# Kernel tuning notes

Hardware: AMD Instinct MI355X
Metric: run time of the kernel (lower is better)

## Reference

```python
import jax, jax.numpy as jnp
import numpy as np

H = 16       # num heads
D = 80       # head dim
HID = H * D  # 1280
S = 4096     # total tokens


def setup_inputs() -> dict:
    key = jax.random.key(0)
    ks = jax.random.split(key, 6)
    x = jax.random.normal(ks[0], (S, HID), dtype=jnp.float32)
    # 4 images of 1024 patch tokens each
    cu_seqlens = jnp.array([0, 1024, 2048, 3072, 4096], dtype=jnp.int32)
    rotary_pos_emb = jax.random.normal(ks[1], (S, D // 2), dtype=jnp.float32)
    sc = 1.0 / np.sqrt(HID)
    qkv_w = jax.random.normal(ks[2], (3 * HID, HID), dtype=jnp.float32) * sc
    qkv_b = jax.random.normal(ks[3], (3 * HID,), dtype=jnp.float32) * 0.02
    proj_w = jax.random.normal(ks[4], (HID, HID), dtype=jnp.float32) * sc
    proj_b = jax.random.normal(ks[5], (HID,), dtype=jnp.float32) * 0.02
    return {"x": x, "cu_seqlens": cu_seqlens, "rotary_pos_emb": rotary_pos_emb,
            "qkv_w": qkv_w, "qkv_b": qkv_b, "proj_w": proj_w, "proj_b": proj_b}


def _rotate_half(t):
    t1, t2 = jnp.split(t, 2, axis=-1)
    return jnp.concatenate([-t2, t1], axis=-1)


def _apply_rope(t, freqs):
    # t: [S, H, D], freqs: [S, D//2] -> cos/sin broadcast as [S, 1, D]
    emb = jnp.concatenate([freqs, freqs], axis=-1)[:, None, :]
    return t * jnp.cos(emb) + _rotate_half(t) * jnp.sin(emb)


def reference(x, cu_seqlens, rotary_pos_emb, qkv_w, qkv_b, proj_w, proj_b):
    seq_len = x.shape[0]
    qkv = (x @ qkv_w.T + qkv_b).reshape(seq_len, 3, H, D)
    q, k, v = qkv[:, 0], qkv[:, 1], qkv[:, 2]  # each [S, H, D]
    q = _apply_rope(q, rotary_pos_emb)
    k = _apply_rope(k, rotary_pos_emb)
    # block-diagonal mask from cu_seqlens: same segment -> 0, else dtype min
    seg = jnp.searchsorted(cu_seqlens[1:], jnp.arange(seq_len), side='right')
    neg = jnp.finfo(q.dtype).min
    attn_mask = jnp.where(seg[:, None] == seg[None, :], 0.0, neg).astype(q.dtype)
    scores = jnp.einsum('shd,thd->hst', q, k) / jnp.sqrt(jnp.asarray(D, q.dtype))
    scores = scores + attn_mask[None]
    attn = jax.nn.softmax(scores.astype(jnp.float32), axis=-1).astype(q.dtype)
    out = jnp.einsum('hst,thd->shd', attn, v).reshape(seq_len, H * D)
    return out @ proj_w.T + proj_b
```

## Files before the change

### kernel.cpp

```cpp
#include <hip/hip_runtime.h>

typedef _Float16 f16;
typedef __attribute__((ext_vector_type(8))) _Float16 f16x8;
typedef __attribute__((ext_vector_type(4))) float f32x4;

#define SEQ   4096
#define NH    16
#define HD    80
#define HIDN  1280
#define DP    96

#define KSZ   3328
#define VSZ   4480
#define HSZ   (2*KSZ + 2*VSZ)

#define KQ   1280
#define NQ   3840
#define NIT  10

__device__ __forceinline__ void gload16(const void* g, void* l) {
  __builtin_amdgcn_global_load_lds(
      (const __attribute__((address_space(1))) unsigned int*)g,
      (__attribute__((address_space(3))) unsigned int*)l, 16, 0, 0);
}

__device__ __forceinline__ f16x8 bc16(uint4 u) { return __builtin_bit_cast(f16x8, u); }
__device__ __forceinline__ unsigned pk2(float a, float b) {
  return __builtin_bit_cast(unsigned, __builtin_amdgcn_cvt_pkrtz(a, b));
}

#define BAR() __builtin_amdgcn_s_barrier()
#define VMCNT(n) do { asm volatile("s_waitcnt vmcnt(" #n ")" ::: "memory"); \
                      __builtin_amdgcn_sched_barrier(0); } while (0)
#define STG(Lb, g, buf, h, kt)                                                  \
  do {                                                                          \
    gload16((g) + (size_t)((h) * 128) * KQ + (kt) * 64,                         \
            (Lb) + (buf) * 16384 + ((h) * 128) * 64 + w * 512);                 \
    gload16((g) + (size_t)((h) * 128 + 64) * KQ + (kt) * 64,                    \
            (Lb) + (buf) * 16384 + ((h) * 128 + 64) * 64 + w * 512);            \
  } while (0)
#define MFQ(IOFF, JOFF, BB)                                                     \
  do {                                                                          \
    __builtin_amdgcn_s_setprio(1);                                              \
    _Pragma("unroll")                                                           \
    for (int i_ = 0; i_ < 4; i_++)                                              \
      _Pragma("unroll")                                                         \
      for (int j_ = 0; j_ < 2; j_++)                                            \
        _Pragma("unroll")                                                       \
        for (int s_ = 0; s_ < 2; s_++)                                          \
          acc[i_ + IOFF][j_ + JOFF] = __builtin_amdgcn_mfma_f32_16x16x32_f16(   \
              a[i_][s_], BB[j_][s_], acc[i_ + IOFF][j_ + JOFF], 0, 0, 0);       \
    __builtin_amdgcn_s_setprio(0);                                              \
  } while (0)

__global__ __launch_bounds__(256) void cvt3_kernel(const float* __restrict__ s0,
                                                   const float* __restrict__ s1,
                                                   const float* __restrict__ s2,
                                                   f16* __restrict__ d0,
                                                   f16* __restrict__ d1,
                                                   f16* __restrict__ d2,
                                                   int n0, int n1, int n2) {
  long i = (long)(blockIdx.x * 256 + threadIdx.x) * 8;
  const float* s; f16* d;
  if (i < n0)                { s = s0 + i;            d = d0 + i; }
  else if (i < n0 + n1)      { s = s1 + (i - n0);     d = d1 + (i - n0); }
  else if (i < n0 + n1 + n2) { s = s2 + (i - n0 - n1); d = d2 + (i - n0 - n1); }
  else return;
  f32x4 v0 = *(const f32x4*)(s);
  f32x4 v1 = *(const f32x4*)(s + 4);
  f16x8 o;
#pragma unroll
  for (int j = 0; j < 4; j++) { o[j] = (f16)v0[j]; o[4 + j] = (f16)v1[j]; }
  *(f16x8*)(d) = o;
}

__global__ __launch_bounds__(512, 2) void qkv_gemm8(const f16* __restrict__ A,
                                                    const f16* __restrict__ B,
                                                    const float* __restrict__ bias,
                                                    f16* __restrict__ C) {
  __shared__ __align__(16) f16 LA[2 * 16384];
  __shared__ __align__(16) f16 LB[2 * 16384];
  const int tid = threadIdx.x, w = tid >> 6, l = tid & 63;
  const int bid = (blockIdx.x & 7) * 30 + (blockIdx.x >> 3);
  const int bx = bid % 15, by = bid / 15;
  const int m0 = by * 256, n0 = bx * 256;
  const int wm = (w >> 2) * 128, wn = (w & 3) * 64;
  const int fr = l & 15, fq = l >> 4;
  const int rx = fr & 7;
  const int cA0 = (fq ^ rx) * 8;
  const int cA1 = ((4 + fq) ^ rx) * 8;

  const int srow = w * 8 + (l >> 3);
  const int scol = ((l & 7) ^ (l >> 3)) * 8;
  const f16* gA = A + (size_t)(m0 + srow) * KQ + scol;
  const f16* gB = B + (size_t)(n0 + srow) * KQ + scol;

  f32x4 acc[8][4] = {};
  f16x8 a[4][2], b0[2][2], b1[2][2];

  STG(LA, gA, 0, 0, 0); STG(LA, gA, 0, 1, 0);
  STG(LB, gB, 0, 0, 0); STG(LB, gB, 0, 1, 0);
  STG(LB, gB, 1, 0, 1); STG(LB, gB, 1, 1, 1);
  VMCNT(4);
  BAR();

  for (int it = 0; it < NIT; ++it) {
    const int t = 2 * it;
    const bool lastit = (it == NIT - 1);

#pragma unroll
    for (int i = 0; i < 4; i++) {
      a[i][0] = *(const f16x8*)(LA + (wm + i * 16 + fr) * 64 + cA0);
      a[i][1] = *(const f16x8*)(LA + (wm + i * 16 + fr) * 64 + cA1);
    }
#pragma unroll
    for (int j = 0; j < 2; j++) {
      b0[j][0] = *(const f16x8*)(LB + (wn + j * 16 + fr) * 64 + cA0);
      b0[j][1] = *(const f16x8*)(LB + (wn + j * 16 + fr) * 64 + cA1);
    }
    STG(LA, gA, 1, 0, t + 1);
    BAR(); MFQ(0, 0, b0); BAR();

#pragma unroll
    for (int j = 0; j < 2; j++) {
      b1[j][0] = *(const f16x8*)(LB + (wn + 32 + j * 16 + fr) * 64 + cA0);
      b1[j][1] = *(const f16x8*)(LB + (wn + 32 + j * 16 + fr) * 64 + cA1);
    }
    STG(LA, gA, 1, 1, t + 1);
    BAR(); MFQ(0, 2, b1); BAR();

#pragma unroll
    for (int i = 0; i < 4; i++) {
      a[i][0] = *(const f16x8*)(LA + (wm + 64 + i * 16 + fr) * 64 + cA0);
      a[i][1] = *(const f16x8*)(LA + (wm + 64 + i * 16 + fr) * 64 + cA1);
    }
    if (!lastit) { STG(LB, gB, 0, 0, t + 2); }
    BAR(); MFQ(4, 0, b0); BAR();

    if (!lastit) { STG(LB, gB, 0, 1, t + 2); VMCNT(4); }
    else         { VMCNT(0); }
    BAR(); MFQ(4, 2, b1); BAR();

#pragma unroll
    for (int i = 0; i < 4; i++) {
      a[i][0] = *(const f16x8*)(LA + 16384 + (wm + i * 16 + fr) * 64 + cA0);
      a[i][1] = *(const f16x8*)(LA + 16384 + (wm + i * 16 + fr) * 64 + cA1);
    }
#pragma unroll
    for (int j = 0; j < 2; j++) {
      b0[j][0] = *(const f16x8*)(LB + 16384 + (wn + j * 16 + fr) * 64 + cA0);
      b0[j][1] = *(const f16x8*)(LB + 16384 + (wn + j * 16 + fr) * 64 + cA1);
    }
    if (!lastit) { STG(LA, gA, 0, 0, t + 2); }
    BAR(); MFQ(0, 0, b0); BAR();

#pragma unroll
    for (int j = 0; j < 2; j++) {
      b1[j][0] = *(const f16x8*)(LB + 16384 + (wn + 32 + j * 16 + fr) * 64 + cA0);
      b1[j][1] = *(const f16x8*)(LB + 16384 + (wn + 32 + j * 16 + fr) * 64 + cA1);
    }
    if (!lastit) { STG(LA, gA, 0, 1, t + 2); }
    BAR(); MFQ(0, 2, b1); BAR();

#pragma unroll
    for (int i = 0; i < 4; i++) {
      a[i][0] = *(const f16x8*)(LA + 16384 + (wm + 64 + i * 16 + fr) * 64 + cA0);
      a[i][1] = *(const f16x8*)(LA + 16384 + (wm + 64 + i * 16 + fr) * 64 + cA1);
    }
    if (!lastit) { STG(LB, gB, 1, 0, t + 3); }
    BAR(); MFQ(4, 0, b0); BAR();

    if (!lastit) { STG(LB, gB, 1, 1, t + 3); VMCNT(4); }
    BAR(); MFQ(4, 2, b1); BAR();
  }

#pragma unroll
  for (int i = 0; i < 8; i++) {
    const int row = m0 + wm + i * 16 + fq * 4;
#pragma unroll
    for (int j = 0; j < 4; j++) {
      const int col = n0 + wn + j * 16 + fr;
      const float bv = bias[col];
#pragma unroll
      for (int q = 0; q < 4; q++)
        C[(size_t)(row + q) * NQ + col] = (f16)(acc[i][j][q] + bv);
    }
  }
}

template<int OUT_F32>
__global__ __launch_bounds__(256) void gemm_bt(const f16* __restrict__ A,
                                               const f16* __restrict__ B,
                                               const float* __restrict__ bias,
                                               void* __restrict__ C,
                                               int M, int N, int K) {
  __shared__ __align__(16) f16 As[128 * 32];
  __shared__ __align__(16) f16 Bs[128 * 32];
  const int tid = threadIdx.x;
  const int w = tid >> 6, l = tid & 63;
  const int m0 = blockIdx.y * 128, n0 = blockIdx.x * 128;
  const int wm = (w >> 1) * 64, wn = (w & 1) * 64;

  const int c0 = w * 64 + l;
  const int c1 = (4 + w) * 64 + l;
  const size_t a0 = (size_t)(m0 + (c0 >> 2)) * K + (c0 & 3) * 8;
  const size_t a1 = (size_t)(m0 + (c1 >> 2)) * K + (c1 & 3) * 8;
  const size_t b0 = (size_t)(n0 + (c0 >> 2)) * K + (c0 & 3) * 8;
  const size_t b1 = (size_t)(n0 + (c1 >> 2)) * K + (c1 & 3) * 8;

  f32x4 acc[4][4] = {};
  const int fr = l & 15, fg = (l >> 4) * 8;

  for (int k0 = 0; k0 < K; k0 += 32) {
    if (k0) __syncthreads();
    gload16(A + a0 + k0, As + w * 512);
    gload16(A + a1 + k0, As + (4 + w) * 512);
    gload16(B + b0 + k0, Bs + w * 512);
    gload16(B + b1 + k0, Bs + (4 + w) * 512);
    __syncthreads();
    f16x8 af[4], bf[4];
#pragma unroll
    for (int i = 0; i < 4; i++)
      af[i] = *(const f16x8*)(As + (wm + i * 16 + fr) * 32 + fg);
#pragma unroll
    for (int j = 0; j < 4; j++)
      bf[j] = *(const f16x8*)(Bs + (wn + j * 16 + fr) * 32 + fg);
#pragma unroll
    for (int i = 0; i < 4; i++)
#pragma unroll
      for (int j = 0; j < 4; j++)
        acc[i][j] = __builtin_amdgcn_mfma_f32_16x16x32_f16(af[i], bf[j], acc[i][j], 0, 0, 0);
  }

  const int q4 = (l >> 4) * 4;
#pragma unroll
  for (int i = 0; i < 4; i++) {
    const int row = m0 + wm + i * 16 + q4;
#pragma unroll
    for (int j = 0; j < 4; j++) {
      const int col = n0 + wn + j * 16 + fr;
      const float bv = bias[col];
#pragma unroll
      for (int q = 0; q < 4; q++) {
        float v = acc[i][j][q] + bv;
        if (OUT_F32) ((float*)C)[(size_t)(row + q) * N + col] = v;
        else         ((f16*)C)[(size_t)(row + q) * N + col] = (f16)v;
      }
    }
  }
}

__global__ __launch_bounds__(256) void rope_kernel(const f16* __restrict__ qkvb,
                                                   const float* __restrict__ rpe,
                                                   f16* __restrict__ qh,
                                                   f16* __restrict__ kh) {
  const float SCLT = 0.1118033988749895f * 1.4426950408889634f;
  int t = blockIdx.x * 256 + threadIdx.x;
  if (t >= SEQ * NH * 40) return;
  const int d = t % 40;
  const int h = (t / 40) % NH;
  const int s = t / (40 * NH);
  const float f = rpe[s * 40 + d];
  float sn, cs;
  __sincosf(f, &sn, &cs);
  const size_t base = (size_t)s * (3 * HIDN) + h * HD;
  const float q0 = (float)qkvb[base + d];
  const float q1 = (float)qkvb[base + 40 + d];
  const float k0 = (float)qkvb[base + HIDN + d];
  const float k1 = (float)qkvb[base + HIDN + 40 + d];
  const size_t ob = ((size_t)h * SEQ + s) * DP;
  qh[ob + d]      = (f16)((q0 * cs - q1 * sn) * SCLT);
  qh[ob + 40 + d] = (f16)((q1 * cs + q0 * sn) * SCLT);
  kh[ob + d]      = (f16)(k0 * cs - k1 * sn);
  kh[ob + 40 + d] = (f16)(k1 * cs + k0 * sn);
  if (d < DP - HD) { qh[ob + HD + d] = (f16)0.f; kh[ob + HD + d] = (f16)0.f; }
}

__global__ __launch_bounds__(256) void vtrans_kernel(const f16* __restrict__ qkvb,
                                                     f16* __restrict__ vt) {
  __shared__ f16 tile[HD][65];
  const int h = blockIdx.y;
  const int s0 = blockIdx.x * 64;
  for (int idx = threadIdx.x; idx < 64 * HD; idx += 256) {
    const int sr = idx / HD, d = idx % HD;
    tile[d][sr] = qkvb[(size_t)(s0 + sr) * (3 * HIDN) + 2 * HIDN + h * HD + d];
  }
  __syncthreads();
  for (int idx = threadIdx.x; idx < HD * 64; idx += 256) {
    const int d = idx >> 6, sc = idx & 63;
    const int b = sc >> 5, s = sc & 31, g = s >> 3, j = s & 7;
    const int act = b * 32 + ((j < 4) ? (4 * g + j) : (16 + 4 * g + (j - 4)));
    vt[((size_t)h * HD + d) * SEQ + s0 + sc] = tile[d][act];
  }
}

__global__ __launch_bounds__(512, 4) void attn_kernel(const f16* __restrict__ qh,
                                                      const f16* __restrict__ kh,
                                                      const f16* __restrict__ vt,
                                                      const int* __restrict__ cu,
                                                      f16* __restrict__ ao) {
  __shared__ __align__(16) f16 smem[2 * HSZ];
  const int tid = threadIdx.x, w = tid >> 6, l = tid & 63;
  const int grp = w >> 2, wq = w & 3;
  const int h = blockIdx.y;
  const int qblk = blockIdx.x * 128;
  int seg = 0;
  while (cu[seg + 1] <= qblk) seg++;
  const int kvb = cu[seg], kve = cu[seg + 1];
  const int nt = (kve - kvb + 63) >> 6;
  const int fr = l & 15, fg = (l >> 4) * 8;
  const int row0 = qblk + wq * 32;

  const f16* qb = qh + ((size_t)h * SEQ + row0 + fr) * DP + fg;
  f16x8 aq0[3], aq1[3];
#pragma unroll
  for (int kk = 0; kk < 3; kk++) {
    aq0[kk] = *(const f16x8*)(qb + kk * 32);
    aq1[kk] = *(const f16x8*)(qb + 16 * DP + kk * 32);
  }

  const int k0g = tid / 384, k0r = (tid % 384) / 12, k0c = tid % 12;
  const int k1r = (128 + tid) / 12, k1c = (128 + tid) % 12;
  const int v0g = tid / 320, v0r = (tid % 320) / 4, v0c = tid & 3;
  const int v1r = (192 + tid) >> 2, v1c = (192 + tid) & 3;
  const f16* kp0 = kh + ((size_t)h * SEQ + kvb + k0g * 32 + k0r) * DP + k0c * 8;
  const f16* kp1 = kh + ((size_t)h * SEQ + kvb + 32 + k1r) * DP + k1c * 8;
  const f16* vp0 = vt + ((size_t)h * HD + v0r) * SEQ + kvb + v0g * 32 + v0c * 8;
  const f16* vp1 = vt + ((size_t)h * HD + v1r) * SEQ + kvb + 32 + v1c * 8;
  const int dK0 = k0g * KSZ + k0r * 104 + k0c * 8;
  const int dK1 = KSZ + k1r * 104 + k1c * 8;
  const int dV0 = 2 * KSZ + v0g * VSZ + v0r * 56 + v0c * 8;
  const int dV1 = 2 * KSZ + VSZ + v1r * 56 + v1c * 8;

  float m = -1e30f, ls0 = 0.f, ls1 = 0.f;
  f32x4 o0[5] = {}, o1[5] = {};

  uint4 rk0, rk1, rv0, rv1;
  rk0 = *(const uint4*)kp0;
  if (tid < 256) rk1 = *(const uint4*)kp1;
  rv0 = *(const uint4*)vp0;
  if (tid < 128) rv1 = *(const uint4*)vp1;
  *(uint4*)(smem + dK0) = rk0;
  if (tid < 256) *(uint4*)(smem + dK1) = rk1;
  *(uint4*)(smem + dV0) = rv0;
  if (tid < 128) *(uint4*)(smem + dV1) = rv1;
  __syncthreads();

  for (int t = 0; t < nt; t++) {
    const int p = t & 1;
    const int off = (t + 1) * 64;
    const bool more = (t + 1 < nt);

    if (more) {
      rk0 = *(const uint4*)(kp0 + (size_t)off * DP);
      if (tid < 256) rk1 = *(const uint4*)(kp1 + (size_t)off * DP);
      rv0 = *(const uint4*)(vp0 + off);
      if (tid < 128) rv1 = *(const uint4*)(vp1 + off);
    }

    const f16* myK = smem + p * HSZ + grp * KSZ;
    const f16* myV = smem + p * HSZ + 2 * KSZ + grp * VSZ;

    f32x4 s00 = {0.f,0.f,0.f,0.f}, s10 = {0.f,0.f,0.f,0.f};
    f32x4 s01 = {0.f,0.f,0.f,0.f}, s11 = {0.f,0.f,0.f,0.f};
    __builtin_amdgcn_s_setprio(1);
#pragma unroll
    for (int kk = 0; kk < 3; kk++) {
      const f16x8 k0 = *(const f16x8*)(myK + fr * 104 + kk * 32 + fg);
      const f16x8 k1 = *(const f16x8*)(myK + (16 + fr) * 104 + kk * 32 + fg);
      s00 = __builtin_amdgcn_mfma_f32_16x16x32_f16(k0, aq0[kk], s00, 0, 0, 0);
      s10 = __builtin_amdgcn_mfma_f32_16x16x32_f16(k1, aq0[kk], s10, 0, 0, 0);
      s01 = __builtin_amdgcn_mfma_f32_16x16x32_f16(k0, aq1[kk], s01, 0, 0, 0);
      s11 = __builtin_amdgcn_mfma_f32_16x16x32_f16(k1, aq1[kk], s11, 0, 0, 0);
    }
    __builtin_amdgcn_s_setprio(0);

    float pmax = fmaxf(fmaxf(s00[0], s10[0]), fmaxf(s01[0], s11[0]));
#pragma unroll
    for (int j = 1; j < 4; j++) {
      pmax = fmaxf(pmax, fmaxf(s00[j], s10[j]));
      pmax = fmaxf(pmax, fmaxf(s01[j], s11[j]));
    }
    if (__any(pmax > m + 8.f)) {
      float tmax = pmax;
      tmax = fmaxf(tmax, __shfl_xor(tmax, 1));
      tmax = fmaxf(tmax, __shfl_xor(tmax, 2));
      tmax = fmaxf(tmax, __shfl_xor(tmax, 4));
      tmax = fmaxf(tmax, __shfl_xor(tmax, 8));
      tmax = fmaxf(tmax, __shfl_xor(tmax, 16));
      tmax = fmaxf(tmax, __shfl_xor(tmax, 32));
      const float aa = __builtin_amdgcn_exp2f(m - tmax);
      m = tmax;
      ls0 *= aa; ls1 *= aa;
#pragma unroll
      for (int dt = 0; dt < 5; dt++)
#pragma unroll
        for (int j = 0; j < 4; j++) { o0[dt][j] *= aa; o1[dt][j] *= aa; }
    }

#pragma unroll
    for (int r = 0; r < 4; r++) {
      s00[r] = __builtin_amdgcn_exp2f(s00[r] - m);
      s10[r] = __builtin_amdgcn_exp2f(s10[r] - m);
      s01[r] = __builtin_amdgcn_exp2f(s01[r] - m);
      s11[r] = __builtin_amdgcn_exp2f(s11[r] - m);
      ls0 += s00[r] + s10[r];
      ls1 += s01[r] + s11[r];
    }
    uint4 ua, ub;
    ua.x = pk2(s00[0], s00[1]); ua.y = pk2(s00[2], s00[3]);
    ua.z = pk2(s10[0], s10[1]); ua.w = pk2(s10[2], s10[3]);
    ub.x = pk2(s01[0], s01[1]); ub.y = pk2(s01[2], s01[3]);
    ub.z = pk2(s11[0], s11[1]); ub.w = pk2(s11[2], s11[3]);
    const f16x8 paA = bc16(ua), paB = bc16(ub);

    __builtin_amdgcn_s_setprio(1);
#pragma unroll
    for (int dt = 0; dt < 5; dt++) {
      const f16x8 bv = *(const f16x8*)(myV + (dt * 16 + fr) * 56 + fg);
      o0[dt] = __builtin_amdgcn_mfma_f32_16x16x32_f16(paA, bv, o0[dt], 0, 0, 0);
      o1[dt] = __builtin_amdgcn_mfma_f32_16x16x32_f16(paB, bv, o1[dt], 0, 0, 0);
    }
    __builtin_amdgcn_s_setprio(0);

    if (more) {
      f16* dst = smem + (1 - p) * HSZ;
      *(uint4*)(dst + dK0) = rk0;
      if (tid < 256) *(uint4*)(dst + dK1) = rk1;
      *(uint4*)(dst + dV0) = rv0;
      if (tid < 128) *(uint4*)(dst + dV1) = rv1;
    }
    __syncthreads();
  }

  ls0 += __shfl_xor(ls0, 16); ls0 += __shfl_xor(ls0, 32);
  ls1 += __shfl_xor(ls1, 16); ls1 += __shfl_xor(ls1, 32);

  float* mb = (float*)smem;
  if (grp == 1) {
    float* dst = mb + (wq * 64 + l) * 43;
    dst[0] = m; dst[1] = ls0; dst[2] = ls1;
#pragma unroll
    for (int dt = 0; dt < 5; dt++)
#pragma unroll
      for (int j = 0; j < 4; j++) {
        dst[3 + dt * 4 + j]  = o0[dt][j];
        dst[23 + dt * 4 + j] = o1[dt][j];
      }
  }
  __syncthreads();
  if (grp == 0) {
    const float* src = mb + (wq * 64 + l) * 43;
    const float mB = src[0];
    const float M = fmaxf(m, mB);
    const float aA = __builtin_amdgcn_exp2f(m - M);
    const float aB = __builtin_amdgcn_exp2f(mB - M);
    ls0 = ls0 * aA + src[1] * aB;
    ls1 = ls1 * aA + src[2] * aB;
#pragma unroll
    for (int dt = 0; dt < 5; dt++)
#pragma unroll
      for (int j = 0; j < 4; j++) {
        o0[dt][j] = o0[dt][j] * aA + src[3 + dt * 4 + j] * aB;
        o1[dt][j] = o1[dt][j] * aA + src[23 + dt * 4 + j] * aB;
      }

    const float inv0 = 1.0f / ls0, inv1 = 1.0f / ls1;
    float iv0[4], iv1[4];
#pragma unroll
    for (int j = 0; j < 4; j++) {
      const int srcl = (l & 48) | ((l >> 4) * 4 + j);
      iv0[j] = __shfl(inv0, srcl);
      iv1[j] = __shfl(inv1, srcl);
    }
    const int orow = row0 + (l >> 4) * 4;
#pragma unroll
    for (int dt = 0; dt < 5; dt++)
#pragma unroll
      for (int j = 0; j < 4; j++) {
        ao[(size_t)(orow + j) * HIDN + h * HD + dt * 16 + fr]      = (f16)(o0[dt][j] * iv0[j]);
        ao[(size_t)(orow + 16 + j) * HIDN + h * HD + dt * 16 + fr] = (f16)(o1[dt][j] * iv1[j]);
      }
  }
}

extern "C" void kernel_launch(void* const* d_in, const int* in_sizes, int n_in,
                              void* d_out, int out_size, void* d_ws, size_t ws_size,
                              hipStream_t stream) {
  const float* x      = (const float*)d_in[0];
  const int*   cu     = (const int*)d_in[1];
  const float* rpe    = (const float*)d_in[2];
  const float* qkv_w  = (const float*)d_in[3];
  const float* qkv_b  = (const float*)d_in[4];
  const float* proj_w = (const float*)d_in[5];
  const float* proj_b = (const float*)d_in[6];

  char* ws = (char*)d_ws;
  f16* xb    = (f16*)(ws);
  f16* wqkv  = (f16*)(ws + 10485760);
  f16* wproj = (f16*)(ws + 20316160);
  f16* qkvb  = (f16*)(ws + 23592960);
  f16* qh    = (f16*)(ws + 55050240);
  f16* kh    = (f16*)(ws + 67633152);
  f16* vt    = (f16*)(ws + 80216064);
  f16* ao    = xb;

  const int n0 = SEQ * HIDN, n1 = 3 * HIDN * HIDN, n2 = HIDN * HIDN;
  cvt3_kernel<<<(n0 + n1 + n2) / (256 * 8), 256, 0, stream>>>(
      x, qkv_w, proj_w, xb, wqkv, wproj, n0, n1, n2);

  qkv_gemm8<<<240, 512, 0, stream>>>(xb, wqkv, qkv_b, qkvb);

  rope_kernel<<<(SEQ * NH * 40) / 256, 256, 0, stream>>>(qkvb, rpe, qh, kh);
  vtrans_kernel<<<dim3(SEQ / 64, NH), 256, 0, stream>>>(qkvb, vt);

  attn_kernel<<<dim3(SEQ / 128, NH), 512, 0, stream>>>(qh, kh, vt, cu, ao);

  gemm_bt<1><<<dim3(HIDN / 128, SEQ / 128), 256, 0, stream>>>(
      ao, wproj, proj_b, d_out, SEQ, HIDN, HIDN);
}
```

Baseline: 154.3 us.

## Widen attention to three KV groups with async LDS loads, fuse rope/vtrans, deepen proj GEMM K-tile

The attention kernel moves from 2 to 3 key/value groups (768 threads, 96-key tiles) and stages K/V straight into LDS with global_load_lds instead of register round-trips. The three partial softmax states are then merged in two phases. RoPE and the V transpose are fused into one prep kernel with vectorized 8-wide rope, and the output projection GEMM now loads 64-wide K slices per barrier. The goal is fewer launches, fewer barriers and better latency hiding. The costs are a higher register and LDS budget per block, clamped loads on a partial last tile, and a longer merge.

```diff
diff --git a/kernel.cpp b/kernel.cpp
--- a/kernel.cpp
+++ b/kernel.cpp
@@ -10,9 +10,10 @@
 #define HIDN  1280
 #define DP    96
 
-#define KSZ   3328
-#define VSZ   4480
-#define HSZ   (2*KSZ + 2*VSZ)
+#define KTS   3072
+#define VTS   2560
+#define KREG  (3*KTS)
+#define ABUF  (KREG + 3*VTS)
 
 #define KQ   1280
 #define NQ   3840
@@ -24,10 +25,10 @@
       (__attribute__((address_space(3))) unsigned int*)l, 16, 0, 0);
 }
 
-__device__ __forceinline__ f16x8 bc16(uint4 u) { return __builtin_bit_cast(f16x8, u); }
 __device__ __forceinline__ unsigned pk2(float a, float b) {
   return __builtin_bit_cast(unsigned, __builtin_amdgcn_cvt_pkrtz(a, b));
 }
+__device__ __forceinline__ f16x8 bc16(uint4 u) { return __builtin_bit_cast(f16x8, u); }
 
 #define BAR() __builtin_amdgcn_s_barrier()
 #define VMCNT(n) do { asm volatile("s_waitcnt vmcnt(" #n ")" ::: "memory"); \
@@ -189,47 +190,53 @@
 }
 
 template<int OUT_F32>
-__global__ __launch_bounds__(256) void gemm_bt(const f16* __restrict__ A,
-                                               const f16* __restrict__ B,
-                                               const float* __restrict__ bias,
-                                               void* __restrict__ C,
-                                               int M, int N, int K) {
-  __shared__ __align__(16) f16 As[128 * 32];
-  __shared__ __align__(16) f16 Bs[128 * 32];
+__global__ __launch_bounds__(256) void gemm_bt64(const f16* __restrict__ A,
+                                                 const f16* __restrict__ B,
+                                                 const float* __restrict__ bias,
+                                                 void* __restrict__ C,
+                                                 int M, int N, int K) {
+  __shared__ __align__(16) f16 AsF[8192];
+  __shared__ __align__(16) f16 BsF[8192];
   const int tid = threadIdx.x;
   const int w = tid >> 6, l = tid & 63;
   const int m0 = blockIdx.y * 128, n0 = blockIdx.x * 128;
   const int wm = (w >> 1) * 64, wn = (w & 1) * 64;
-
-  const int c0 = w * 64 + l;
-  const int c1 = (4 + w) * 64 + l;
-  const size_t a0 = (size_t)(m0 + (c0 >> 2)) * K + (c0 & 3) * 8;
-  const size_t a1 = (size_t)(m0 + (c1 >> 2)) * K + (c1 & 3) * 8;
-  const size_t b0 = (size_t)(n0 + (c0 >> 2)) * K + (c0 & 3) * 8;
-  const size_t b1 = (size_t)(n0 + (c1 >> 2)) * K + (c1 & 3) * 8;
+  const int fr = l & 15, fg = (l >> 4) * 8;
+
+  size_t aoff[4], boff[4];
+#pragma unroll
+  for (int i = 0; i < 4; i++) {
+    const int d = i * 256 + tid;
+    const int sub = d >> 9, dd = d & 511;
+    const int r = dd >> 2, c = (dd & 3) + sub * 4;
+    aoff[i] = (size_t)(m0 + r) * K + c * 8;
+    boff[i] = (size_t)(n0 + r) * K + c * 8;
+  }
 
   f32x4 acc[4][4] = {};
-  const int fr = l & 15, fg = (l >> 4) * 8;
-
-  for (int k0 = 0; k0 < K; k0 += 32) {
+
+  for (int k0 = 0; k0 < K; k0 += 64) {
     if (k0) __syncthreads();
-    gload16(A + a0 + k0, As + w * 512);
-    gload16(A + a1 + k0, As + (4 + w) * 512);
-    gload16(B + b0 + k0, Bs + w * 512);
-    gload16(B + b1 + k0, Bs + (4 + w) * 512);
+#pragma unroll
+    for (int i = 0; i < 4; i++) gload16(A + aoff[i] + k0, AsF + (i * 256 + tid) * 8);
+#pragma unroll
+    for (int i = 0; i < 4; i++) gload16(B + boff[i] + k0, BsF + (i * 256 + tid) * 8);
     __syncthreads();
-    f16x8 af[4], bf[4];
+    f16x8 af[4][2], bf[4][2];
 #pragma unroll
     for (int i = 0; i < 4; i++)
-      af[i] = *(const f16x8*)(As + (wm + i * 16 + fr) * 32 + fg);
-#pragma unroll
-    for (int j = 0; j < 4; j++)
-      bf[j] = *(const f16x8*)(Bs + (wn + j * 16 + fr) * 32 + fg);
+#pragma unroll
+      for (int s = 0; s < 2; s++) {
+        af[i][s] = *(const f16x8*)(AsF + s * 4096 + (wm + i * 16 + fr) * 32 + fg);
+        bf[i][s] = *(const f16x8*)(BsF + s * 4096 + (wn + i * 16 + fr) * 32 + fg);
+      }
 #pragma unroll
     for (int i = 0; i < 4; i++)
 #pragma unroll
       for (int j = 0; j < 4; j++)
-        acc[i][j] = __builtin_amdgcn_mfma_f32_16x16x32_f16(af[i], bf[j], acc[i][j], 0, 0, 0);
+#pragma unroll
+        for (int s = 0; s < 2; s++)
+          acc[i][j] = __builtin_amdgcn_mfma_f32_16x16x32_f16(af[i][s], bf[j][s], acc[i][j], 0, 0, 0);
   }
 
   const int q4 = (l >> 4) * 4;
@@ -250,56 +257,74 @@
   }
 }
 
-__global__ __launch_bounds__(256) void rope_kernel(const f16* __restrict__ qkvb,
+#define RPB 1280
+__global__ __launch_bounds__(256) void prep_kernel(const f16* __restrict__ qkvb,
                                                    const float* __restrict__ rpe,
                                                    f16* __restrict__ qh,
-                                                   f16* __restrict__ kh) {
-  const float SCLT = 0.1118033988749895f * 1.4426950408889634f;
-  int t = blockIdx.x * 256 + threadIdx.x;
-  if (t >= SEQ * NH * 40) return;
-  const int d = t % 40;
-  const int h = (t / 40) % NH;
-  const int s = t / (40 * NH);
-  const float f = rpe[s * 40 + d];
-  float sn, cs;
-  __sincosf(f, &sn, &cs);
-  const size_t base = (size_t)s * (3 * HIDN) + h * HD;
-  const float q0 = (float)qkvb[base + d];
-  const float q1 = (float)qkvb[base + 40 + d];
-  const float k0 = (float)qkvb[base + HIDN + d];
-  const float k1 = (float)qkvb[base + HIDN + 40 + d];
-  const size_t ob = ((size_t)h * SEQ + s) * DP;
-  qh[ob + d]      = (f16)((q0 * cs - q1 * sn) * SCLT);
-  qh[ob + 40 + d] = (f16)((q1 * cs + q0 * sn) * SCLT);
-  kh[ob + d]      = (f16)(k0 * cs - k1 * sn);
-  kh[ob + 40 + d] = (f16)(k1 * cs + k0 * sn);
-  if (d < DP - HD) { qh[ob + HD + d] = (f16)0.f; kh[ob + HD + d] = (f16)0.f; }
-}
-
-__global__ __launch_bounds__(256) void vtrans_kernel(const f16* __restrict__ qkvb,
-                                                     f16* __restrict__ vt) {
+                                                   f16* __restrict__ kh,
+                                                   f16* __restrict__ vt) {
   __shared__ f16 tile[HD][65];
-  const int h = blockIdx.y;
-  const int s0 = blockIdx.x * 64;
-  for (int idx = threadIdx.x; idx < 64 * HD; idx += 256) {
-    const int sr = idx / HD, d = idx % HD;
-    tile[d][sr] = qkvb[(size_t)(s0 + sr) * (3 * HIDN) + 2 * HIDN + h * HD + d];
-  }
-  __syncthreads();
-  for (int idx = threadIdx.x; idx < HD * 64; idx += 256) {
-    const int d = idx >> 6, sc = idx & 63;
-    const int b = sc >> 5, s = sc & 31, g = s >> 3, j = s & 7;
-    const int act = b * 32 + ((j < 4) ? (4 * g + j) : (16 + 4 * g + (j - 4)));
-    vt[((size_t)h * HD + d) * SEQ + s0 + sc] = tile[d][act];
-  }
-}
-
-__global__ __launch_bounds__(512, 4) void attn_kernel(const f16* __restrict__ qh,
+  const int b = blockIdx.x;
+  if (b < RPB) {
+    const float SCLT = 0.1118033988749895f * 1.4426950408889634f;
+    const int t = b * 256 + threadIdx.x;
+    const int d8 = (t % 5) * 8;
+    const int h = (t / 5) % NH;
+    const int s = t / (5 * NH);
+    const f32x4 f0 = *(const f32x4*)(rpe + s * 40 + d8);
+    const f32x4 f1 = *(const f32x4*)(rpe + s * 40 + d8 + 4);
+    const f16* base = qkvb + (size_t)s * (3 * HIDN) + h * HD;
+    const f16x8 q0 = *(const f16x8*)(base + d8);
+    const f16x8 q1 = *(const f16x8*)(base + 40 + d8);
+    const f16x8 k0 = *(const f16x8*)(base + HIDN + d8);
+    const f16x8 k1 = *(const f16x8*)(base + HIDN + 40 + d8);
+    f16x8 oq0, oq1, ok0, ok1;
+#pragma unroll
+    for (int j = 0; j < 8; j++) {
+      const float fv = (j < 4) ? f0[j] : f1[j - 4];
+      float sn, cs;
+      __sincosf(fv, &sn, &cs);
+      const float a = (float)q0[j], bq = (float)q1[j];
+      oq0[j] = (f16)((a * cs - bq * sn) * SCLT);
+      oq1[j] = (f16)((bq * cs + a * sn) * SCLT);
+      const float ka = (float)k0[j], kb = (float)k1[j];
+      ok0[j] = (f16)(ka * cs - kb * sn);
+      ok1[j] = (f16)(kb * cs + ka * sn);
+    }
+    const size_t ob = ((size_t)h * SEQ + s) * DP;
+    *(f16x8*)(qh + ob + d8)      = oq0;
+    *(f16x8*)(qh + ob + 40 + d8) = oq1;
+    *(f16x8*)(kh + ob + d8)      = ok0;
+    *(f16x8*)(kh + ob + 40 + d8) = ok1;
+    if (d8 == 32) {
+      const f16x8 z = {};
+      *(f16x8*)(qh + ob + 80) = z; *(f16x8*)(qh + ob + 88) = z;
+      *(f16x8*)(kh + ob + 80) = z; *(f16x8*)(kh + ob + 88) = z;
+    }
+  } else {
+    const int bb = b - RPB;
+    const int h = bb >> 6;
+    const int s0 = (bb & 63) * 64;
+    for (int idx = threadIdx.x; idx < 64 * HD; idx += 256) {
+      const int sr = idx / HD, d = idx % HD;
+      tile[d][sr] = qkvb[(size_t)(s0 + sr) * (3 * HIDN) + 2 * HIDN + h * HD + d];
+    }
+    __syncthreads();
+    for (int idx = threadIdx.x; idx < HD * 64; idx += 256) {
+      const int d = idx >> 6, sc = idx & 63;
+      const int blk = sc >> 5, s = sc & 31, g = s >> 3, j = s & 7;
+      const int act = blk * 32 + ((j < 4) ? (4 * g + j) : (16 + 4 * g + (j - 4)));
+      vt[((size_t)h * HD + d) * SEQ + s0 + sc] = tile[d][act];
+    }
+  }
+}
+
+__global__ __launch_bounds__(768, 6) void attn_kernel(const f16* __restrict__ qh,
                                                       const f16* __restrict__ kh,
                                                       const f16* __restrict__ vt,
                                                       const int* __restrict__ cu,
                                                       f16* __restrict__ ao) {
-  __shared__ __align__(16) f16 smem[2 * HSZ];
+  __shared__ __align__(16) f16 smem[2 * ABUF];
   const int tid = threadIdx.x, w = tid >> 6, l = tid & 63;
   const int grp = w >> 2, wq = w & 3;
   const int h = blockIdx.y;
@@ -307,7 +332,7 @@
   int seg = 0;
   while (cu[seg + 1] <= qblk) seg++;
   const int kvb = cu[seg], kve = cu[seg + 1];
-  const int nt = (kve - kvb + 63) >> 6;
+  const int nt = (kve - kvb + 95) / 96;
   const int fr = l & 15, fg = (l >> 4) * 8;
   const int row0 = qblk + wq * 32;
 
@@ -319,116 +344,111 @@
     aq1[kk] = *(const f16x8*)(qb + 16 * DP + kk * 32);
   }
 
-  const int k0g = tid / 384, k0r = (tid % 384) / 12, k0c = tid % 12;
-  const int k1r = (128 + tid) / 12, k1c = (128 + tid) % 12;
-  const int v0g = tid / 320, v0r = (tid % 320) / 4, v0c = tid & 3;
-  const int v1r = (192 + tid) >> 2, v1c = (192 + tid) & 3;
-  const f16* kp0 = kh + ((size_t)h * SEQ + kvb + k0g * 32 + k0r) * DP + k0c * 8;
-  const f16* kp1 = kh + ((size_t)h * SEQ + kvb + 32 + k1r) * DP + k1c * 8;
-  const f16* vp0 = vt + ((size_t)h * HD + v0r) * SEQ + kvb + v0g * 32 + v0c * 8;
-  const f16* vp1 = vt + ((size_t)h * HD + v1r) * SEQ + kvb + 32 + v1c * 8;
-  const int dK0 = k0g * KSZ + k0r * 104 + k0c * 8;
-  const int dK1 = KSZ + k1r * 104 + k1c * 8;
-  const int dV0 = 2 * KSZ + v0g * VSZ + v0r * 56 + v0c * 8;
-  const int dV1 = 2 * KSZ + VSZ + v1r * 56 + v1c * 8;
+  const int kr0 = tid / 12, kc0 = (tid % 12) * 8;
+  const int kr1 = (768 + tid) / 12, kc1 = ((768 + tid) % 12) * 8;
+  const int vg0 = tid / 320, vr0 = (tid % 320) / 4, vc0 = (tid & 3) * 8;
+  const int vg1 = (768 + tid) / 320, vr1 = ((768 + tid) % 320) / 4, vc1 = (tid & 3) * 8;
+  const f16* kbase = kh + (size_t)h * SEQ * DP;
+  const f16* vbase = vt + (size_t)h * HD * SEQ;
 
   float m = -1e30f, ls0 = 0.f, ls1 = 0.f;
   f32x4 o0[5] = {}, o1[5] = {};
 
-  uint4 rk0, rk1, rv0, rv1;
-  rk0 = *(const uint4*)kp0;
-  if (tid < 256) rk1 = *(const uint4*)kp1;
-  rv0 = *(const uint4*)vp0;
-  if (tid < 128) rv1 = *(const uint4*)vp1;
-  *(uint4*)(smem + dK0) = rk0;
-  if (tid < 256) *(uint4*)(smem + dK1) = rk1;
-  *(uint4*)(smem + dV0) = rv0;
-  if (tid < 128) *(uint4*)(smem + dV1) = rv1;
+  auto stage = [&](int buf, int t) {
+    f16* Kd = smem + buf * ABUF;
+    f16* Vd = Kd + KREG;
+    const int rb = kvb + t * 96;
+    {
+      const int r = min(rb + kr0, SEQ - 1);
+      gload16(kbase + (size_t)r * DP + kc0, Kd + tid * 8);
+    }
+    if (tid < 384) {
+      const int r = min(rb + kr1, SEQ - 1);
+      gload16(kbase + (size_t)r * DP + kc1, Kd + (768 + tid) * 8);
+    }
+    {
+      const int c = min(rb + vg0 * 32 + vc0, SEQ - 8);
+      gload16(vbase + (size_t)vr0 * SEQ + c, Vd + tid * 8);
+    }
+    if (tid < 192) {
+      const int c = min(rb + vg1 * 32 + vc1, SEQ - 8);
+      gload16(vbase + (size_t)vr1 * SEQ + c, Vd + (768 + tid) * 8);
+    }
+  };
+
+  stage(0, 0);
   __syncthreads();
 
   for (int t = 0; t < nt; t++) {
     const int p = t & 1;
-    const int off = (t + 1) * 64;
-    const bool more = (t + 1 < nt);
-
-    if (more) {
-      rk0 = *(const uint4*)(kp0 + (size_t)off * DP);
-      if (tid < 256) rk1 = *(const uint4*)(kp1 + (size_t)off * DP);
-      rv0 = *(const uint4*)(vp0 + off);
-      if (tid < 128) rv1 = *(const uint4*)(vp1 + off);
-    }
-
-    const f16* myK = smem + p * HSZ + grp * KSZ;
-    const f16* myV = smem + p * HSZ + 2 * KSZ + grp * VSZ;
-
-    f32x4 s00 = {0.f,0.f,0.f,0.f}, s10 = {0.f,0.f,0.f,0.f};
-    f32x4 s01 = {0.f,0.f,0.f,0.f}, s11 = {0.f,0.f,0.f,0.f};
-    __builtin_amdgcn_s_setprio(1);
-#pragma unroll
-    for (int kk = 0; kk < 3; kk++) {
-      const f16x8 k0 = *(const f16x8*)(myK + fr * 104 + kk * 32 + fg);
-      const f16x8 k1 = *(const f16x8*)(myK + (16 + fr) * 104 + kk * 32 + fg);
-      s00 = __builtin_amdgcn_mfma_f32_16x16x32_f16(k0, aq0[kk], s00, 0, 0, 0);
-      s10 = __builtin_amdgcn_mfma_f32_16x16x32_f16(k1, aq0[kk], s10, 0, 0, 0);
-      s01 = __builtin_amdgcn_mfma_f32_16x16x32_f16(k0, aq1[kk], s01, 0, 0, 0);
-      s11 = __builtin_amdgcn_mfma_f32_16x16x32_f16(k1, aq1[kk], s11, 0, 0, 0);
-    }
-    __builtin_amdgcn_s_setprio(0);
-
-    float pmax = fmaxf(fmaxf(s00[0], s10[0]), fmaxf(s01[0], s11[0]));
-#pragma unroll
-    for (int j = 1; j < 4; j++) {
-      pmax = fmaxf(pmax, fmaxf(s00[j], s10[j]));
-      pmax = fmaxf(pmax, fmaxf(s01[j], s11[j]));
-    }
-    if (__any(pmax > m + 8.f)) {
-      float tmax = pmax;
-      tmax = fmaxf(tmax, __shfl_xor(tmax, 1));
-      tmax = fmaxf(tmax, __shfl_xor(tmax, 2));
-      tmax = fmaxf(tmax, __shfl_xor(tmax, 4));
-      tmax = fmaxf(tmax, __shfl_xor(tmax, 8));
-      tmax = fmaxf(tmax, __shfl_xor(tmax, 16));
-      tmax = fmaxf(tmax, __shfl_xor(tmax, 32));
-      const float aa = __builtin_amdgcn_exp2f(m - tmax);
-      m = tmax;
-      ls0 *= aa; ls1 *= aa;
-#pragma unroll
-      for (int dt = 0; dt < 5; dt++)
-#pragma unroll
-        for (int j = 0; j < 4; j++) { o0[dt][j] *= aa; o1[dt][j] *= aa; }
-    }
-
-#pragma unroll
-    for (int r = 0; r < 4; r++) {
-      s00[r] = __builtin_amdgcn_exp2f(s00[r] - m);
-      s10[r] = __builtin_amdgcn_exp2f(s10[r] - m);
-      s01[r] = __builtin_amdgcn_exp2f(s01[r] - m);
-      s11[r] = __builtin_amdgcn_exp2f(s11[r] - m);
-      ls0 += s00[r] + s10[r];
-      ls1 += s01[r] + s11[r];
-    }
-    uint4 ua, ub;
-    ua.x = pk2(s00[0], s00[1]); ua.y = pk2(s00[2], s00[3]);
-    ua.z = pk2(s10[0], s10[1]); ua.w = pk2(s10[2], s10[3]);
-    ub.x = pk2(s01[0], s01[1]); ub.y = pk2(s01[2], s01[3]);
-    ub.z = pk2(s11[0], s11[1]); ub.w = pk2(s11[2], s11[3]);
-    const f16x8 paA = bc16(ua), paB = bc16(ub);
-
-    __builtin_amdgcn_s_setprio(1);
-#pragma unroll
-    for (int dt = 0; dt < 5; dt++) {
-      const f16x8 bv = *(const f16x8*)(myV + (dt * 16 + fr) * 56 + fg);
-      o0[dt] = __builtin_amdgcn_mfma_f32_16x16x32_f16(paA, bv, o0[dt], 0, 0, 0);
-      o1[dt] = __builtin_amdgcn_mfma_f32_16x16x32_f16(paB, bv, o1[dt], 0, 0, 0);
-    }
-    __builtin_amdgcn_s_setprio(0);
-
-    if (more) {
-      f16* dst = smem + (1 - p) * HSZ;
-      *(uint4*)(dst + dK0) = rk0;
-      if (tid < 256) *(uint4*)(dst + dK1) = rk1;
-      *(uint4*)(dst + dV0) = rv0;
-      if (tid < 128) *(uint4*)(dst + dV1) = rv1;
+    if (t + 1 < nt) stage(1 - p, t + 1);
+
+    const int cur = kvb + t * 96 + grp * 32;
+    if (cur < kve) {
+      const f16* myK = smem + p * ABUF + grp * KTS;
+      const f16* myV = smem + p * ABUF + KREG + grp * VTS;
+
+      f32x4 s00 = {0.f,0.f,0.f,0.f}, s10 = {0.f,0.f,0.f,0.f};
+      f32x4 s01 = {0.f,0.f,0.f,0.f}, s11 = {0.f,0.f,0.f,0.f};
+      __builtin_amdgcn_s_setprio(1);
+#pragma unroll
+      for (int kk = 0; kk < 3; kk++) {
+        const f16x8 k0 = *(const f16x8*)(myK + fr * 96 + kk * 32 + fg);
+        const f16x8 k1 = *(const f16x8*)(myK + (16 + fr) * 96 + kk * 32 + fg);
+        s00 = __builtin_amdgcn_mfma_f32_16x16x32_f16(k0, aq0[kk], s00, 0, 0, 0);
+        s10 = __builtin_amdgcn_mfma_f32_16x16x32_f16(k1, aq0[kk], s10, 0, 0, 0);
+        s01 = __builtin_amdgcn_mfma_f32_16x16x32_f16(k0, aq1[kk], s01, 0, 0, 0);
+        s11 = __builtin_amdgcn_mfma_f32_16x16x32_f16(k1, aq1[kk], s11, 0, 0, 0);
+      }
+      __builtin_amdgcn_s_setprio(0);
+
+      float pmax = fmaxf(fmaxf(s00[0], s10[0]), fmaxf(s01[0], s11[0]));
+#pragma unroll
+      for (int j = 1; j < 4; j++) {
+        pmax = fmaxf(pmax, fmaxf(s00[j], s10[j]));
+        pmax = fmaxf(pmax, fmaxf(s01[j], s11[j]));
+      }
+      if (__any(pmax > m + 8.f)) {
+        float tmax = pmax;
+        tmax = fmaxf(tmax, __shfl_xor(tmax, 1));
+        tmax = fmaxf(tmax, __shfl_xor(tmax, 2));
+        tmax = fmaxf(tmax, __shfl_xor(tmax, 4));
+        tmax = fmaxf(tmax, __shfl_xor(tmax, 8));
+        tmax = fmaxf(tmax, __shfl_xor(tmax, 16));
+        tmax = fmaxf(tmax, __shfl_xor(tmax, 32));
+        const float aa = __builtin_amdgcn_exp2f(m - tmax);
+        m = tmax;
+        ls0 *= aa; ls1 *= aa;
+#pragma unroll
+        for (int dt = 0; dt < 5; dt++)
+#pragma unroll
+          for (int j = 0; j < 4; j++) { o0[dt][j] *= aa; o1[dt][j] *= aa; }
+      }
+
+#pragma unroll
+      for (int r = 0; r < 4; r++) {
+        s00[r] = __builtin_amdgcn_exp2f(s00[r] - m);
+        s10[r] = __builtin_amdgcn_exp2f(s10[r] - m);
+        s01[r] = __builtin_amdgcn_exp2f(s01[r] - m);
+        s11[r] = __builtin_amdgcn_exp2f(s11[r] - m);
+        ls0 += s00[r] + s10[r];
+        ls1 += s01[r] + s11[r];
+      }
+      uint4 ua, ub;
+      ua.x = pk2(s00[0], s00[1]); ua.y = pk2(s00[2], s00[3]);
+      ua.z = pk2(s10[0], s10[1]); ua.w = pk2(s10[2], s10[3]);
+      ub.x = pk2(s01[0], s01[1]); ub.y = pk2(s01[2], s01[3]);
+      ub.z = pk2(s11[0], s11[1]); ub.w = pk2(s11[2], s11[3]);
+      const f16x8 paA = bc16(ua), paB = bc16(ub);
+
+      __builtin_amdgcn_s_setprio(1);
+#pragma unroll
+      for (int dt = 0; dt < 5; dt++) {
+        const f16x8 bv = *(const f16x8*)(myV + (dt * 16 + fr) * 32 + fg);
+        o0[dt] = __builtin_amdgcn_mfma_f32_16x16x32_f16(paA, bv, o0[dt], 0, 0, 0);
+        o1[dt] = __builtin_amdgcn_mfma_f32_16x16x32_f16(paB, bv, o1[dt], 0, 0, 0);
+      }
+      __builtin_amdgcn_s_setprio(0);
     }
     __syncthreads();
   }
@@ -437,34 +457,42 @@
   ls1 += __shfl_xor(ls1, 16); ls1 += __shfl_xor(ls1, 32);
 
   float* mb = (float*)smem;
-  if (grp == 1) {
-    float* dst = mb + (wq * 64 + l) * 43;
-    dst[0] = m; dst[1] = ls0; dst[2] = ls1;
-#pragma unroll
-    for (int dt = 0; dt < 5; dt++)
-#pragma unroll
-      for (int j = 0; j < 4; j++) {
-        dst[3 + dt * 4 + j]  = o0[dt][j];
-        dst[23 + dt * 4 + j] = o1[dt][j];
-      }
-  }
-  __syncthreads();
+#pragma unroll
+  for (int ph = 0; ph < 2; ph++) {
+    const int src_grp = 2 - ph;
+    if (grp == src_grp) {
+      float* dst = mb + (wq * 64 + l) * 43;
+      dst[0] = m; dst[1] = ls0; dst[2] = ls1;
+#pragma unroll
+      for (int dt = 0; dt < 5; dt++)
+#pragma unroll
+        for (int j = 0; j < 4; j++) {
+          dst[3 + dt * 4 + j]  = o0[dt][j];
+          dst[23 + dt * 4 + j] = o1[dt][j];
+        }
+    }
+    __syncthreads();
+    if (grp == 0) {
+      const float* src = mb + (wq * 64 + l) * 43;
+      const float mB = src[0];
+      const float M = fmaxf(m, mB);
+      const float aA = __builtin_amdgcn_exp2f(m - M);
+      const float aB = __builtin_amdgcn_exp2f(mB - M);
+      m = M;
+      ls0 = ls0 * aA + src[1] * aB;
+      ls1 = ls1 * aA + src[2] * aB;
+#pragma unroll
+      for (int dt = 0; dt < 5; dt++)
+#pragma unroll
+        for (int j = 0; j < 4; j++) {
+          o0[dt][j] = o0[dt][j] * aA + src[3 + dt * 4 + j] * aB;
+          o1[dt][j] = o1[dt][j] * aA + src[23 + dt * 4 + j] * aB;
+        }
+    }
+    __syncthreads();
+  }
+
   if (grp == 0) {
-    const float* src = mb + (wq * 64 + l) * 43;
-    const float mB = src[0];
-    const float M = fmaxf(m, mB);
-    const float aA = __builtin_amdgcn_exp2f(m - M);
-    const float aB = __builtin_amdgcn_exp2f(mB - M);
-    ls0 = ls0 * aA + src[1] * aB;
-    ls1 = ls1 * aA + src[2] * aB;
-#pragma unroll
-    for (int dt = 0; dt < 5; dt++)
-#pragma unroll
-      for (int j = 0; j < 4; j++) {
-        o0[dt][j] = o0[dt][j] * aA + src[3 + dt * 4 + j] * aB;
-        o1[dt][j] = o1[dt][j] * aA + src[23 + dt * 4 + j] * aB;
-      }
-
     const float inv0 = 1.0f / ls0, inv1 = 1.0f / ls1;
     float iv0[4], iv1[4];
 #pragma unroll
@@ -511,11 +539,10 @@
 
   qkv_gemm8<<<240, 512, 0, stream>>>(xb, wqkv, qkv_b, qkvb);
 
-  rope_kernel<<<(SEQ * NH * 40) / 256, 256, 0, stream>>>(qkvb, rpe, qh, kh);
-  vtrans_kernel<<<dim3(SEQ / 64, NH), 256, 0, stream>>>(qkvb, vt);
-
-  attn_kernel<<<dim3(SEQ / 128, NH), 512, 0, stream>>>(qh, kh, vt, cu, ao);
-
-  gemm_bt<1><<<dim3(HIDN / 128, SEQ / 128), 256, 0, stream>>>(
+  prep_kernel<<<RPB + 1024, 256, 0, stream>>>(qkvb, rpe, qh, kh, vt);
+
+  attn_kernel<<<dim3(SEQ / 128, NH), 768, 0, stream>>>(qh, kh, vt, cu, ao);
+
+  gemm_bt64<1><<<dim3(HIDN / 128, SEQ / 128), 256, 0, stream>>>(
       ao, wproj, proj_b, d_out, SEQ, HIDN, HIDN);
 }
```

Result: slower. 222.4 us (+44.2%).
